# Kernel tuning notes

Measured on AMD Instinct MI355X. Metric: run time of the kernel, lower is better.

## Reference

```python
import jax, jax.numpy as jnp
import numpy as np

ALPHA = 0.2          # LeakyReLU negative slope
NEG_INF = -9e15      # mask value used by the original module


def setup_inputs() -> dict:
    key = jax.random.key(0)
    k1, k2, k3, k4 = jax.random.split(key, 4)
    N, Din, Dout = 8192, 512, 256
    features = jax.random.normal(k1, (N, Din), dtype=jnp.float32)
    adj = jax.random.randint(k2, (N, N), 0, 2, dtype=jnp.int32)
    W = jax.random.normal(k3, (Din, Dout), dtype=jnp.float32) * (1.414 / np.sqrt(Din))
    a = jax.random.normal(k4, (2 * Dout, 1), dtype=jnp.float32) * (1.414 / np.sqrt(2 * Dout))
    return {"features": features, "adj": adj, "W": W, "a": a}


def reference(features, adj, W, a):
    Dout = W.shape[1]
    Wh = features @ W                       # [N, Dout]
    # e_ij = leakyrelu([Wh_i || Wh_j] @ a) decomposes additively:
    # identical math to the N*N*2D concat in the original, without materializing it.
    src = Wh @ a[:Dout, 0]                  # [N]  contribution of node i
    dst = Wh @ a[Dout:, 0]                  # [N]  contribution of node j
    e = jax.nn.leaky_relu(src[:, None] + dst[None, :], negative_slope=ALPHA)  # [N, N]
    masked = jnp.where(adj > 0, e, NEG_INF)
    attention = jax.nn.softmax(masked, axis=1)   # dropout p=0.0 (eval) -> identity
    h_prime = attention @ Wh                # [N, Dout]
    return jax.nn.elu(h_prime)
```

## Files before the change

kernel.cpp:

```cpp
#include <hip/hip_runtime.h>
#include <hip/hip_bf16.h>

#define NN   8192
#define DIN  512
#define DOUT 256

typedef __attribute__((ext_vector_type(8)))  short s16x8;
typedef __attribute__((ext_vector_type(16))) float f32x16;

static __device__ __forceinline__ unsigned short f2bf(float f) {
    union { float f; unsigned u; } v; v.f = f;
    unsigned r = v.u + 0x7fffu + ((v.u >> 16) & 1u);
    return (unsigned short)(r >> 16);
}

__global__ __launch_bounds__(256) void k_wh3(const float* __restrict__ feat,
                                             const float* __restrict__ W,
                                             const float* __restrict__ a,
                                             uint4* __restrict__ Bpk,
                                             float* __restrict__ src,
                                             float* __restrict__ dst) {
    __shared__ float lf[16 * DIN];
    __shared__ float red[2][4][16];
    const int tid = threadIdx.x;
    const int i0  = blockIdx.x * 16;
    const int w   = tid >> 6, lane = tid & 63;

    const float4* fsrc = (const float4*)(feat + (size_t)i0 * DIN);
    float4* fdst = (float4*)lf;
    #pragma unroll
    for (int q = 0; q < 8; ++q) fdst[tid + q * 256] = fsrc[tid + q * 256];
    __syncthreads();

    const int c = tid;
    float outs[16];
    #pragma unroll
    for (int r = 0; r < 16; ++r) outs[r] = 0.f;

    for (int k = 0; k < DIN; k += 4) {
        float w0 = W[(k + 0) * DOUT + c];
        float w1 = W[(k + 1) * DOUT + c];
        float w2 = W[(k + 2) * DOUT + c];
        float w3 = W[(k + 3) * DOUT + c];
        #pragma unroll
        for (int r = 0; r < 16; ++r) {
            float4 f = *(const float4*)&lf[r * DIN + k];
            outs[r] = fmaf(f.x, w0, fmaf(f.y, w1, fmaf(f.z, w2, fmaf(f.w, w3, outs[r]))));
        }
    }

    unsigned short tb[16];
    #pragma unroll
    for (int r = 0; r < 16; ++r) tb[r] = f2bf(outs[r]);
    const int ct = c >> 5, l31c = c & 31;
    Bpk[((size_t)ct * 512 + blockIdx.x) * 64 +  0 + l31c] = *(uint4*)&tb[0];
    Bpk[((size_t)ct * 512 + blockIdx.x) * 64 + 32 + l31c] = *(uint4*)&tb[8];

    const float as_ = a[c], ad_ = a[DOUT + c];
    #pragma unroll
    for (int r = 0; r < 16; ++r) {
        float s = outs[r] * as_;
        float d = outs[r] * ad_;
        #pragma unroll
        for (int off = 32; off; off >>= 1) {
            s += __shfl_xor(s, off);
            d += __shfl_xor(d, off);
        }
        if (lane == 0) { red[0][w][r] = s; red[1][w][r] = d; }
    }
    __syncthreads();
    if (tid < 16)
        src[i0 + tid] = red[0][0][tid] + red[0][1][tid] + red[0][2][tid] + red[0][3][tid];
    else if (tid < 32) {
        int r = tid - 16;
        dst[i0 + r] = red[1][0][r] + red[1][1][r] + red[1][2][r] + red[1][3][r];
    }
}

__global__ __launch_bounds__(256) void k_mask(const int* __restrict__ adj,
                                              unsigned char* __restrict__ bits) {
    const int row = blockIdx.x;
    const int tid = threadIdx.x;
    const int* base = adj + (size_t)row * NN + tid * 32;
    unsigned int u = 0;
    #pragma unroll
    for (int j = 0; j < 8; ++j) {
        int4 v = *(const int4*)(base + j * 4);
        unsigned int b = (v.x > 0 ? 1u : 0u) | (v.y > 0 ? 2u : 0u) |
                         (v.z > 0 ? 4u : 0u) | (v.w > 0 ? 8u : 0u);
        u |= b << (j * 4);
    }
    *(unsigned int*)(bits + (size_t)row * 1024 + tid * 4) = u;
}

__global__ __launch_bounds__(256, 2) void k_attn11(const unsigned char* __restrict__ bits,
                                                   const uint4* __restrict__ Bpk,
                                                   const float* __restrict__ src,
                                                   const float* __restrict__ dstg,
                                                   float* __restrict__ denp,
                                                   float* __restrict__ part) {
    const int tid  = threadIdx.x;
    const int lane = tid & 63;
    const int wv   = tid >> 6;
    const int l31  = lane & 31, lhi = lane >> 5;
    const int lhi8 = lhi * 8;
    const int rowg = wv & 1, colg = wv >> 1;

    const int ks   = blockIdx.x & 7;
    const int rt   = blockIdx.x >> 3;
    const int ktg0 = ks * 64;

    const int gr0 = rt * 128 + rowg * 64 + l31;
    const int gr1 = gr0 + 32;
    const float si0 = src[gr0], si1 = src[gr1];
    const unsigned long long* bq0 =
        (const unsigned long long*)(bits + (size_t)gr0 * 1024 + ks * 128);
    const unsigned long long* bq1 =
        (const unsigned long long*)(bits + (size_t)gr1 * 1024 + ks * 128);
    const float* dk = dstg + ks * 1024 + lhi8;

    f32x16 acc[2][4];
    #pragma unroll
    for (int a = 0; a < 2; ++a)
        #pragma unroll
        for (int c = 0; c < 4; ++c)
            #pragma unroll
            for (int e = 0; e < 16; ++e) acc[a][c][e] = 0.f;
    float den0 = 0.f, den1 = 0.f;

    for (int tt = 0; tt < 16; ++tt) {
        const unsigned long long m0 = bq0[tt];
        const unsigned long long m1 = bq1[tt];
        #pragma unroll
        for (int q = 0; q < 4; ++q) {
            const int t = tt * 4 + q;
            s16x8 bf[4];
            #pragma unroll
            for (int c = 0; c < 4; ++c) {
                uint4 v = Bpk[((size_t)(colg * 4 + c) * 512 + ktg0 + t) * 64 + lane];
                bf[c] = *(s16x8*)&v;
            }
            float4 d0 = *(const float4*)(dk + t * 16);
            float4 d1 = *(const float4*)(dk + t * 16 + 4);
            const float df[8] = {d0.x, d0.y, d0.z, d0.w, d1.x, d1.y, d1.z, d1.w};
            const unsigned int m8_0 = (unsigned int)(m0 >> (q * 16 + lhi8)) & 0xffu;
            const unsigned int m8_1 = (unsigned int)(m1 >> (q * 16 + lhi8)) & 0xffu;
            s16x8 pa0, pa1;
            #pragma unroll
            for (int jj = 0; jj < 8; ++jj) {
                float x0 = si0 + df[jj];
                x0 = fmaxf(x0, 0.2f * x0);
                float p0 = (m8_0 >> jj) & 1u ? __expf(x0) : 0.f;
                den0 += p0;
                pa0[jj] = (short)f2bf(p0);
                float x1 = si1 + df[jj];
                x1 = fmaxf(x1, 0.2f * x1);
                float p1 = (m8_1 >> jj) & 1u ? __expf(x1) : 0.f;
                den1 += p1;
                pa1[jj] = (short)f2bf(p1);
            }
            __builtin_amdgcn_s_setprio(1);
            #pragma unroll
            for (int c = 0; c < 4; ++c) {
                acc[0][c] = __builtin_amdgcn_mfma_f32_32x32x16_bf16(pa0, bf[c], acc[0][c], 0, 0, 0);
                acc[1][c] = __builtin_amdgcn_mfma_f32_32x32x16_bf16(pa1, bf[c], acc[1][c], 0, 0, 0);
            }
            __builtin_amdgcn_s_setprio(0);
        }
    }

    den0 += __shfl_xor(den0, 32);
    den1 += __shfl_xor(den1, 32);
    if (colg == 0 && lhi == 0) {
        denp[(size_t)ks * NN + gr0] = den0;
        denp[(size_t)ks * NN + gr1] = den1;
    }

    float* pp = part + (size_t)ks * (NN * DOUT);
    #pragma unroll
    for (int a = 0; a < 2; ++a) {
        #pragma unroll
        for (int c = 0; c < 4; ++c) {
            #pragma unroll
            for (int e = 0; e < 16; ++e) {
                const int row = rt * 128 + rowg * 64 + a * 32 + (e & 3) + 8 * (e >> 2) + 4 * lhi;
                const int col = colg * 128 + c * 32 + l31;
                pp[(size_t)row * DOUT + col] = acc[a][c][e];
            }
        }
    }
}

__global__ __launch_bounds__(256) void k_finish3(const float* __restrict__ part,
                                                 const float* __restrict__ denp,
                                                 float* __restrict__ out) {
    const int idx = blockIdx.x * 256 + threadIdx.x;
    const int row = idx >> 6;
    float den = 0.f;
    #pragma unroll
    for (int i = 0; i < 8; ++i) den += denp[(size_t)i * NN + row];
    float rv = den > 0.f ? 1.f / den : 0.f;
    const size_t st = (size_t)NN * DOUT / 4;
    const float4* p = (const float4*)part;
    float sx = 0.f, sy = 0.f, sz = 0.f, sw = 0.f;
    #pragma unroll
    for (int i = 0; i < 8; ++i) {
        float4 v = p[idx + i * st];
        sx += v.x; sy += v.y; sz += v.z; sw += v.w;
    }
    float4 s;
    s.x = sx * rv; s.y = sy * rv; s.z = sz * rv; s.w = sw * rv;
    s.x = s.x > 0.f ? s.x : expm1f(s.x);
    s.y = s.y > 0.f ? s.y : expm1f(s.y);
    s.z = s.z > 0.f ? s.z : expm1f(s.z);
    s.w = s.w > 0.f ? s.w : expm1f(s.w);
    ((float4*)out)[idx] = s;
}

extern "C" void kernel_launch(void* const* d_in, const int* in_sizes, int n_in,
                              void* d_out, int out_size, void* d_ws, size_t ws_size,
                              hipStream_t stream) {
    const float* feat = (const float*)d_in[0];
    const int*   adj  = (const int*)d_in[1];
    const float* W    = (const float*)d_in[2];
    const float* a    = (const float*)d_in[3];
    float* out = (float*)d_out;

    char* ws = (char*)d_ws;
    uint4*          Bpk  = (uint4*)ws;
    float*          src  = (float*)(ws + 4194304);
    float*          dst  = (float*)(ws + 4227072);
    float*          denp = (float*)(ws + 4259840);
    unsigned char*  bits = (unsigned char*)(ws + 4521984);
    float*          part = (float*)(ws + 12910592);

    k_mask   <<<8192, 256, 0, stream>>>(adj, bits);
    k_wh3    <<<512,  256, 0, stream>>>(feat, W, a, Bpk, src, dst);
    k_attn11 <<<512,  256, 0, stream>>>(bits, Bpk, src, dst, denp, part);
    k_finish3<<<2048, 256, 0, stream>>>(part, denp, out);
}
```

Before: 222.5 us.

## Merge mask packing with Wh projection and double-buffer B fragments in attention

The adjacency bit-packing and the feature projection now share one launch. Half the blocks pack 32 mask rows each while the other half compute two 16-row Wh tiles, so the memory-bound and compute-bound work can overlap and one launch disappears. The attention kernel also prefetches the next step's Bpk fragments into a second register buffer, so global load latency overlaps the exp and MFMA work. In exchange, register pressure rises, and the projection now runs on only 256 blocks, which may lengthen its critical path.

```diff
diff --git a/kernel.cpp b/kernel.cpp
--- a/kernel.cpp
+++ b/kernel.cpp
@@ -14,86 +14,134 @@
     return (unsigned short)(r >> 16);
 }
 
-__global__ __launch_bounds__(256) void k_wh3(const float* __restrict__ feat,
-                                             const float* __restrict__ W,
-                                             const float* __restrict__ a,
-                                             uint4* __restrict__ Bpk,
-                                             float* __restrict__ src,
-                                             float* __restrict__ dst) {
+__global__ __launch_bounds__(256) void k_prep(const float* __restrict__ feat,
+                                              const float* __restrict__ W,
+                                              const float* __restrict__ a,
+                                              const int* __restrict__ adj,
+                                              uint4* __restrict__ Bpk,
+                                              float* __restrict__ src,
+                                              float* __restrict__ dst,
+                                              unsigned char* __restrict__ bits) {
     __shared__ float lf[16 * DIN];
     __shared__ float red[2][4][16];
     const int tid = threadIdx.x;
-    const int i0  = blockIdx.x * 16;
-    const int w   = tid >> 6, lane = tid & 63;
-
-    const float4* fsrc = (const float4*)(feat + (size_t)i0 * DIN);
-    float4* fdst = (float4*)lf;
-    #pragma unroll
-    for (int q = 0; q < 8; ++q) fdst[tid + q * 256] = fsrc[tid + q * 256];
-    __syncthreads();
-
+
+    if (blockIdx.x < 256) {
+        const int r0 = blockIdx.x * 32;
+        #pragma unroll 4
+        for (int rr = 0; rr < 32; ++rr) {
+            const int row = r0 + rr;
+            const int* base = adj + (size_t)row * NN + tid * 32;
+            unsigned int u = 0;
+            #pragma unroll
+            for (int j = 0; j < 8; ++j) {
+                int4 v = *(const int4*)(base + j * 4);
+                unsigned int b = (v.x > 0 ? 1u : 0u) | (v.y > 0 ? 2u : 0u) |
+                                 (v.z > 0 ? 4u : 0u) | (v.w > 0 ? 8u : 0u);
+                u |= b << (j * 4);
+            }
+            *(unsigned int*)(bits + (size_t)row * 1024 + tid * 4) = u;
+        }
+        return;
+    }
+
+    const int w = tid >> 6, lane = tid & 63;
     const int c = tid;
-    float outs[16];
-    #pragma unroll
-    for (int r = 0; r < 16; ++r) outs[r] = 0.f;
-
-    for (int k = 0; k < DIN; k += 4) {
-        float w0 = W[(k + 0) * DOUT + c];
-        float w1 = W[(k + 1) * DOUT + c];
-        float w2 = W[(k + 2) * DOUT + c];
-        float w3 = W[(k + 3) * DOUT + c];
+    for (int s = 0; s < 2; ++s) {
+        const int i0 = (blockIdx.x - 256) * 32 + s * 16;
+        const int kt = i0 >> 4;
+
+        const float4* fsrc = (const float4*)(feat + (size_t)i0 * DIN);
+        float4* fdst = (float4*)lf;
+        #pragma unroll
+        for (int q = 0; q < 8; ++q) fdst[tid + q * 256] = fsrc[tid + q * 256];
+        __syncthreads();
+
+        float outs[16];
+        #pragma unroll
+        for (int r = 0; r < 16; ++r) outs[r] = 0.f;
+
+        for (int k = 0; k < DIN; k += 4) {
+            float w0 = W[(k + 0) * DOUT + c];
+            float w1 = W[(k + 1) * DOUT + c];
+            float w2 = W[(k + 2) * DOUT + c];
+            float w3 = W[(k + 3) * DOUT + c];
+            #pragma unroll
+            for (int r = 0; r < 16; ++r) {
+                float4 f = *(const float4*)&lf[r * DIN + k];
+                outs[r] = fmaf(f.x, w0, fmaf(f.y, w1, fmaf(f.z, w2, fmaf(f.w, w3, outs[r]))));
+            }
+        }
+
+        unsigned short tb[16];
+        #pragma unroll
+        for (int r = 0; r < 16; ++r) tb[r] = f2bf(outs[r]);
+        const int ct = c >> 5, l31c = c & 31;
+        Bpk[((size_t)ct * 512 + kt) * 64 +  0 + l31c] = *(uint4*)&tb[0];
+        Bpk[((size_t)ct * 512 + kt) * 64 + 32 + l31c] = *(uint4*)&tb[8];
+
+        const float as_ = a[c], ad_ = a[DOUT + c];
         #pragma unroll
         for (int r = 0; r < 16; ++r) {
-            float4 f = *(const float4*)&lf[r * DIN + k];
-            outs[r] = fmaf(f.x, w0, fmaf(f.y, w1, fmaf(f.z, w2, fmaf(f.w, w3, outs[r]))));
-        }
-    }
-
-    unsigned short tb[16];
-    #pragma unroll
-    for (int r = 0; r < 16; ++r) tb[r] = f2bf(outs[r]);
-    const int ct = c >> 5, l31c = c & 31;
-    Bpk[((size_t)ct * 512 + blockIdx.x) * 64 +  0 + l31c] = *(uint4*)&tb[0];
-    Bpk[((size_t)ct * 512 + blockIdx.x) * 64 + 32 + l31c] = *(uint4*)&tb[8];
-
-    const float as_ = a[c], ad_ = a[DOUT + c];
-    #pragma unroll
-    for (int r = 0; r < 16; ++r) {
-        float s = outs[r] * as_;
-        float d = outs[r] * ad_;
-        #pragma unroll
-        for (int off = 32; off; off >>= 1) {
-            s += __shfl_xor(s, off);
-            d += __shfl_xor(d, off);
-        }
-        if (lane == 0) { red[0][w][r] = s; red[1][w][r] = d; }
-    }
-    __syncthreads();
-    if (tid < 16)
-        src[i0 + tid] = red[0][0][tid] + red[0][1][tid] + red[0][2][tid] + red[0][3][tid];
-    else if (tid < 32) {
-        int r = tid - 16;
-        dst[i0 + r] = red[1][0][r] + red[1][1][r] + red[1][2][r] + red[1][3][r];
-    }
-}
-
-__global__ __launch_bounds__(256) void k_mask(const int* __restrict__ adj,
-                                              unsigned char* __restrict__ bits) {
-    const int row = blockIdx.x;
-    const int tid = threadIdx.x;
-    const int* base = adj + (size_t)row * NN + tid * 32;
-    unsigned int u = 0;
-    #pragma unroll
-    for (int j = 0; j < 8; ++j) {
-        int4 v = *(const int4*)(base + j * 4);
-        unsigned int b = (v.x > 0 ? 1u : 0u) | (v.y > 0 ? 2u : 0u) |
-                         (v.z > 0 ? 4u : 0u) | (v.w > 0 ? 8u : 0u);
-        u |= b << (j * 4);
-    }
-    *(unsigned int*)(bits + (size_t)row * 1024 + tid * 4) = u;
-}
-
-__global__ __launch_bounds__(256, 2) void k_attn11(const unsigned char* __restrict__ bits,
+            float sv = outs[r] * as_;
+            float dv = outs[r] * ad_;
+            #pragma unroll
+            for (int off = 32; off; off >>= 1) {
+                sv += __shfl_xor(sv, off);
+                dv += __shfl_xor(dv, off);
+            }
+            if (lane == 0) { red[0][w][r] = sv; red[1][w][r] = dv; }
+        }
+        __syncthreads();
+        if (tid < 16)
+            src[i0 + tid] = red[0][0][tid] + red[0][1][tid] + red[0][2][tid] + red[0][3][tid];
+        else if (tid < 32) {
+            int r = tid - 16;
+            dst[i0 + r] = red[1][0][r] + red[1][1][r] + red[1][2][r] + red[1][3][r];
+        }
+        __syncthreads();
+    }
+}
+
+#define AT12_STEP(Q, TT, BCUR, BNXT, M0, M1)                                             \
+{                                                                                        \
+    const int t_ = (TT) * 4 + (Q);                                                       \
+    if (t_ < 63) {                                        \
+        _Pragma("unroll")                                                                \
+        for (int cc = 0; cc < 4; ++cc) {                                                 \
+            uint4 v_ = Bpk[((size_t)(colg * 4 + cc) * 512 + ktg0 + t_ + 1) * 64 + lane]; \
+            BNXT[cc] = *(s16x8*)&v_;                                                     \
+        }                                                                                \
+    }                                                                                    \
+    float4 d0_ = *(const float4*)(dk + t_ * 16);                                         \
+    float4 d1_ = *(const float4*)(dk + t_ * 16 + 4);                                     \
+    const float df_[8] = {d0_.x, d0_.y, d0_.z, d0_.w, d1_.x, d1_.y, d1_.z, d1_.w};       \
+    const unsigned int m8_0 = (unsigned int)((M0) >> ((Q) * 16 + lhi8)) & 0xffu;         \
+    const unsigned int m8_1 = (unsigned int)((M1) >> ((Q) * 16 + lhi8)) & 0xffu;         \
+    s16x8 pa0_, pa1_;                                                                    \
+    _Pragma("unroll")                                                                    \
+    for (int jj = 0; jj < 8; ++jj) {                                                     \
+        float x0 = si0 + df_[jj];                                                        \
+        x0 = fmaxf(x0, 0.2f * x0);                                   \
+        float p0 = (m8_0 >> jj) & 1u ? __expf(x0) : 0.f;        \
+        den0 += p0;                                                                      \
+        pa0_[jj] = (short)f2bf(p0);                                                      \
+        float x1 = si1 + df_[jj];                                                        \
+        x1 = fmaxf(x1, 0.2f * x1);                                                       \
+        float p1 = (m8_1 >> jj) & 1u ? __expf(x1) : 0.f;                                 \
+        den1 += p1;                                                                      \
+        pa1_[jj] = (short)f2bf(p1);                                                      \
+    }                                                                                    \
+    __builtin_amdgcn_s_setprio(1);                                                       \
+    _Pragma("unroll")                                                                    \
+    for (int cc = 0; cc < 4; ++cc) {                                                     \
+        acc[0][cc] = __builtin_amdgcn_mfma_f32_32x32x16_bf16(pa0_, BCUR[cc], acc[0][cc], 0, 0, 0); \
+        acc[1][cc] = __builtin_amdgcn_mfma_f32_32x32x16_bf16(pa1_, BCUR[cc], acc[1][cc], 0, 0, 0); \
+    }                                                                                    \
+    __builtin_amdgcn_s_setprio(0);                                                       \
+}
+
+__global__ __launch_bounds__(256, 2) void k_attn12(const unsigned char* __restrict__ bits,
                                                    const uint4* __restrict__ Bpk,
                                                    const float* __restrict__ src,
                                                    const float* __restrict__ dstg,
@@ -128,45 +176,20 @@
             for (int e = 0; e < 16; ++e) acc[a][c][e] = 0.f;
     float den0 = 0.f, den1 = 0.f;
 
+    s16x8 bfA[4], bfB[4];
+    #pragma unroll
+    for (int cc = 0; cc < 4; ++cc) {
+        uint4 v = Bpk[((size_t)(colg * 4 + cc) * 512 + ktg0) * 64 + lane];
+        bfA[cc] = *(s16x8*)&v;
+    }
+
     for (int tt = 0; tt < 16; ++tt) {
         const unsigned long long m0 = bq0[tt];
         const unsigned long long m1 = bq1[tt];
-        #pragma unroll
-        for (int q = 0; q < 4; ++q) {
-            const int t = tt * 4 + q;
-            s16x8 bf[4];
-            #pragma unroll
-            for (int c = 0; c < 4; ++c) {
-                uint4 v = Bpk[((size_t)(colg * 4 + c) * 512 + ktg0 + t) * 64 + lane];
-                bf[c] = *(s16x8*)&v;
-            }
-            float4 d0 = *(const float4*)(dk + t * 16);
-            float4 d1 = *(const float4*)(dk + t * 16 + 4);
-            const float df[8] = {d0.x, d0.y, d0.z, d0.w, d1.x, d1.y, d1.z, d1.w};
-            const unsigned int m8_0 = (unsigned int)(m0 >> (q * 16 + lhi8)) & 0xffu;
-            const unsigned int m8_1 = (unsigned int)(m1 >> (q * 16 + lhi8)) & 0xffu;
-            s16x8 pa0, pa1;
-            #pragma unroll
-            for (int jj = 0; jj < 8; ++jj) {
-                float x0 = si0 + df[jj];
-                x0 = fmaxf(x0, 0.2f * x0);
-                float p0 = (m8_0 >> jj) & 1u ? __expf(x0) : 0.f;
-                den0 += p0;
-                pa0[jj] = (short)f2bf(p0);
-                float x1 = si1 + df[jj];
-                x1 = fmaxf(x1, 0.2f * x1);
-                float p1 = (m8_1 >> jj) & 1u ? __expf(x1) : 0.f;
-                den1 += p1;
-                pa1[jj] = (short)f2bf(p1);
-            }
-            __builtin_amdgcn_s_setprio(1);
-            #pragma unroll
-            for (int c = 0; c < 4; ++c) {
-                acc[0][c] = __builtin_amdgcn_mfma_f32_32x32x16_bf16(pa0, bf[c], acc[0][c], 0, 0, 0);
-                acc[1][c] = __builtin_amdgcn_mfma_f32_32x32x16_bf16(pa1, bf[c], acc[1][c], 0, 0, 0);
-            }
-            __builtin_amdgcn_s_setprio(0);
-        }
+        AT12_STEP(0, tt, bfA, bfB, m0, m1);
+        AT12_STEP(1, tt, bfB, bfA, m0, m1);
+        AT12_STEP(2, tt, bfA, bfB, m0, m1);
+        AT12_STEP(3, tt, bfB, bfA, m0, m1);
     }
 
     den0 += __shfl_xor(den0, 32);
@@ -234,8 +257,7 @@
     unsigned char*  bits = (unsigned char*)(ws + 4521984);
     float*          part = (float*)(ws + 12910592);
 
-    k_mask   <<<8192, 256, 0, stream>>>(adj, bits);
-    k_wh3    <<<512,  256, 0, stream>>>(feat, W, a, Bpk, src, dst);
-    k_attn11 <<<512,  256, 0, stream>>>(bits, Bpk, src, dst, denp, part);
+    k_prep   <<<512,  256, 0, stream>>>(feat, W, a, adj, Bpk, src, dst, bits);
+    k_attn12 <<<512,  256, 0, stream>>>(bits, Bpk, src, dst, denp, part);
     k_finish3<<<2048, 256, 0, stream>>>(part, denp, out);
 }
```

New measurement: 268.4 us. +20.6%, slower.
